# Performance work log

Hardware: AMD Instinct MI355X
Metric: run time of the kernel (lower is better)

Reference implementation:

```python
import jax, jax.numpy as jnp
import numpy as np

K = 3  # kernel_size

def setup_inputs() -> dict:
    key = jax.random.key(0)
    k0, k1, k2 = jax.random.split(key, 3)
    B, C, H, W = 8, 128, 128, 128
    x = jax.random.normal(k0, (B, C, H, W), dtype=jnp.float32)
    # kernel_gen params: two 1x1 convs acting on a 1x1 pooled map -> plain matmuls
    w1 = jax.random.normal(k1, (C, C), dtype=jnp.float32) * 0.05          # conv1 weight [out,in]
    b1 = jnp.zeros((C,), dtype=jnp.float32)
    w2 = jax.random.normal(k2, (C * K * K, C), dtype=jnp.float32) * 0.05  # conv2 weight [out,in]
    b2 = jnp.zeros((C * K * K,), dtype=jnp.float32)
    return {"x": x, "w1": w1, "b1": b1, "w2": w2, "b2": b2}

def reference(x, w1, b1, w2, b2):
    B, C, H, W = x.shape
    k = K
    pad = k // 2
    # AdaptiveAvgPool2d(1) -> global mean; 1x1 convs -> matmuls on [B, C]
    pooled = x.mean(axis=(2, 3))                        # [B, C]
    h = jax.nn.relu(pooled @ w1.T + b1)                 # [B, C]
    kern = (h @ w2.T + b2).reshape(B, C, k * k)         # [B, C, k*k], channel-major = reshape(B*C,1,k,k)
    # Dynamic per-sample depthwise conv (cross-correlation, zero pad), via patches
    patches = jax.lax.conv_general_dilated_patches(
        x, (k, k), (1, 1), ((pad, pad), (pad, pad)),
        dimension_numbers=("NCHW", "OIHW", "NCHW"))     # [B, C*k*k, H, W], channel-major over (C, k, k)
    patches = patches.reshape(B, C, k * k, H, W)
    out = jnp.einsum("bcphw,bcp->bchw", patches, kern)  # [B, C, H, W]
    return out
```

## Files before the change

kernel.cpp:

```cpp
#include <hip/hip_runtime.h>

#define BB 8
#define CC 128
#define HH 128
#define WW 128
#define PLANE (HH * WW)
#define KK 9

__global__ __launch_bounds__(256) void pool_kernel(const float* __restrict__ x,
                                                   float* __restrict__ pooled) {
    int bc = blockIdx.x;
    const float4* p4 = (const float4*)(x + (size_t)bc * PLANE);
    int t = threadIdx.x;
    float s = 0.f;
#pragma unroll
    for (int i = 0; i < 16; ++i) {
        float4 v = p4[t + i * 256];
        s += v.x + v.y + v.z + v.w;
    }
#pragma unroll
    for (int off = 32; off > 0; off >>= 1) s += __shfl_down(s, off, 64);
    __shared__ float wsum[4];
    int wave = t >> 6, lane = t & 63;
    if (lane == 0) wsum[wave] = s;
    __syncthreads();
    if (t == 0) {
        float tot = wsum[0] + wsum[1] + wsum[2] + wsum[3];
        pooled[bc] = tot * (1.0f / PLANE);
    }
}

__global__ __launch_bounds__(128) void kerngen_kernel(const float* __restrict__ pooled,
                                                      const float* __restrict__ w1,
                                                      const float* __restrict__ b1,
                                                      const float* __restrict__ w2,
                                                      const float* __restrict__ b2,
                                                      float* __restrict__ kern) {
    int b = blockIdx.x / 9;
    int g = blockIdx.x % 9;
    int j = threadIdx.x;
    __shared__ float ps[CC];
    __shared__ float hs[CC];
    ps[j] = pooled[b * CC + j];
    __syncthreads();
    float acc = b1[j];
    const float* w1r = w1 + j * CC;
#pragma unroll 8
    for (int i = 0; i < CC; ++i) acc += ps[i] * w1r[i];
    hs[j] = fmaxf(acc, 0.f);
    __syncthreads();
    int o = g * CC + j;
    float acc2 = b2[o];
    const float* w2r = w2 + o * CC;
#pragma unroll 8
    for (int i = 0; i < CC; ++i) acc2 += hs[i] * w2r[i];
    kern[b * (CC * KK) + o] = acc2;
}

__global__ __launch_bounds__(256) void conv_kernel(const float* __restrict__ x,
                                                   const float* __restrict__ kern,
                                                   float* __restrict__ out) {
    int bid = blockIdx.x;
    int bc = bid >> 2, slice = bid & 3;
    const float* plane = x + (size_t)bc * PLANE;
    float* oplane = out + (size_t)bc * PLANE;
    const float* wp = kern + (size_t)bc * KK;
    float w[9];
#pragma unroll
    for (int p = 0; p < 9; ++p) w[p] = wp[p];
    int t = threadIdx.x;
#pragma unroll
    for (int i = 0; i < 4; ++i) {
        int q = slice * 1024 + i * 256 + t;
        int y = q >> 5;
        int xq = q & 31;
        int x0 = xq << 2;
        float4 acc = {0.f, 0.f, 0.f, 0.f};
#pragma unroll
        for (int ky = 0; ky < 3; ++ky) {
            int yr = y + ky - 1;
            if (yr < 0 || yr >= HH) continue;
            const float* row = plane + yr * WW;
            float4 c = *(const float4*)(row + x0);
            float l = (x0 > 0) ? row[x0 - 1] : 0.f;
            float r = (xq < 31) ? row[x0 + 4] : 0.f;
            float w0 = w[ky * 3 + 0], w1_ = w[ky * 3 + 1], w2_ = w[ky * 3 + 2];
            acc.x += w0 * l   + w1_ * c.x + w2_ * c.y;
            acc.y += w0 * c.x + w1_ * c.y + w2_ * c.z;
            acc.z += w0 * c.y + w1_ * c.z + w2_ * c.w;
            acc.w += w0 * c.z + w1_ * c.w + w2_ * r;
        }
        *(float4*)(oplane + y * WW + x0) = acc;
    }
}

extern "C" void kernel_launch(void* const* d_in, const int* in_sizes, int n_in,
                              void* d_out, int out_size, void* d_ws, size_t ws_size,
                              hipStream_t stream) {
    const float* x  = (const float*)d_in[0];
    const float* w1 = (const float*)d_in[1];
    const float* b1 = (const float*)d_in[2];
    const float* w2 = (const float*)d_in[3];
    const float* b2 = (const float*)d_in[4];
    float* out = (float*)d_out;

    float* ws = (float*)d_ws;
    float* pooled = ws;
    float* kern   = ws + 1024;

    pool_kernel<<<BB * CC, 256, 0, stream>>>(x, pooled);
    kerngen_kernel<<<BB * 9, 128, 0, stream>>>(pooled, w1, b1, w2, b2, kern);
    conv_kernel<<<BB * CC * 4, 256, 0, stream>>>(x, kern, out);
}
```

Measured before the change: 146.8 us.

## Fuse kernel generation into depthwise conv with rolling row reuse

Removes the separate kernel-generation launch. Each conv block now recomputes the hidden vector and its own 9 taps from the pooled means, using shuffle reductions. The conv now gives each thread an 8-row strip and keeps rolling partial sums, so each input row is loaded once instead of three times. Each block redundantly recomputes the 128x128 first-layer matvec (1024 blocks), which adds L2 traffic and compute before the conv can start.

```diff
diff --git a/kernel.cpp b/kernel.cpp
--- a/kernel.cpp
+++ b/kernel.cpp
@@ -25,72 +25,99 @@
     if (lane == 0) wsum[wave] = s;
     __syncthreads();
     if (t == 0) {
-        float tot = wsum[0] + wsum[1] + wsum[2] + wsum[3];
-        pooled[bc] = tot * (1.0f / PLANE);
+        pooled[bc] = (wsum[0] + wsum[1] + wsum[2] + wsum[3]) * (1.0f / PLANE);
     }
 }
 
-__global__ __launch_bounds__(128) void kerngen_kernel(const float* __restrict__ pooled,
-                                                      const float* __restrict__ w1,
-                                                      const float* __restrict__ b1,
-                                                      const float* __restrict__ w2,
-                                                      const float* __restrict__ b2,
-                                                      float* __restrict__ kern) {
-    int b = blockIdx.x / 9;
-    int g = blockIdx.x % 9;
-    int j = threadIdx.x;
-    __shared__ float ps[CC];
+__global__ __launch_bounds__(512, 4) void fused_conv_kernel(
+        const float* __restrict__ x,
+        const float* __restrict__ pooled,
+        const float* __restrict__ w1,
+        const float* __restrict__ b1,
+        const float* __restrict__ w2,
+        const float* __restrict__ b2,
+        float* __restrict__ out) {
+    int bc = blockIdx.x;
+    int b = bc >> 7;
+    int c = bc & 127;
+    int t = threadIdx.x;
+
     __shared__ float hs[CC];
-    ps[j] = pooled[b * CC + j];
+    __shared__ float ks[KK];
+
+    {
+        int j = t >> 2;
+        int k = t & 3;
+        const float* pr = pooled + b * CC + k * 32;
+        const float* wr = w1 + j * CC + k * 32;
+        float a = 0.f;
+#pragma unroll
+        for (int i = 0; i < 32; ++i) a += pr[i] * wr[i];
+        a += __shfl_down(a, 1, 64);
+        a += __shfl_down(a, 2, 64);
+        if (k == 0) hs[j] = fmaxf(a + b1[j], 0.f);
+    }
     __syncthreads();
-    float acc = b1[j];
-    const float* w1r = w1 + j * CC;
-#pragma unroll 8
-    for (int i = 0; i < CC; ++i) acc += ps[i] * w1r[i];
-    hs[j] = fmaxf(acc, 0.f);
+
+    {
+        int w = t >> 6, lane = t & 63;
+        for (int p = w; p < KK; p += 8) {
+            int o = c * KK + p;
+            const float* wr = w2 + o * CC;
+            float a = hs[lane] * wr[lane] + hs[lane + 64] * wr[lane + 64];
+#pragma unroll
+            for (int off = 32; off > 0; off >>= 1) a += __shfl_down(a, off, 64);
+            if (lane == 0) ks[p] = a + b2[o];
+        }
+    }
     __syncthreads();
-    int o = g * CC + j;
-    float acc2 = b2[o];
-    const float* w2r = w2 + o * CC;
-#pragma unroll 8
-    for (int i = 0; i < CC; ++i) acc2 += hs[i] * w2r[i];
-    kern[b * (CC * KK) + o] = acc2;
-}
 
-__global__ __launch_bounds__(256) void conv_kernel(const float* __restrict__ x,
-                                                   const float* __restrict__ kern,
-                                                   float* __restrict__ out) {
-    int bid = blockIdx.x;
-    int bc = bid >> 2, slice = bid & 3;
+    float w[9];
+#pragma unroll
+    for (int p = 0; p < 9; ++p) w[p] = ks[p];
+
     const float* plane = x + (size_t)bc * PLANE;
     float* oplane = out + (size_t)bc * PLANE;
-    const float* wp = kern + (size_t)bc * KK;
-    float w[9];
+    int xq = t & 31;
+    int x0 = xq << 2;
+    int yb = (t >> 5) * 8;
+
+    float4 A = {0.f, 0.f, 0.f, 0.f};
+    float4 Bv = {0.f, 0.f, 0.f, 0.f};
+
 #pragma unroll
-    for (int p = 0; p < 9; ++p) w[p] = wp[p];
-    int t = threadIdx.x;
-#pragma unroll
-    for (int i = 0; i < 4; ++i) {
-        int q = slice * 1024 + i * 256 + t;
-        int y = q >> 5;
-        int xq = q & 31;
-        int x0 = xq << 2;
-        float4 acc = {0.f, 0.f, 0.f, 0.f};
-#pragma unroll
-        for (int ky = 0; ky < 3; ++ky) {
-            int yr = y + ky - 1;
-            if (yr < 0 || yr >= HH) continue;
+    for (int s = 0; s < 10; ++s) {
+        int yr = yb - 1 + s;
+        float4 cv = {0.f, 0.f, 0.f, 0.f};
+        float l = 0.f, r = 0.f;
+        if (yr >= 0 && yr < HH) {
             const float* row = plane + yr * WW;
-            float4 c = *(const float4*)(row + x0);
-            float l = (x0 > 0) ? row[x0 - 1] : 0.f;
-            float r = (xq < 31) ? row[x0 + 4] : 0.f;
-            float w0 = w[ky * 3 + 0], w1_ = w[ky * 3 + 1], w2_ = w[ky * 3 + 2];
-            acc.x += w0 * l   + w1_ * c.x + w2_ * c.y;
-            acc.y += w0 * c.x + w1_ * c.y + w2_ * c.z;
-            acc.z += w0 * c.y + w1_ * c.z + w2_ * c.w;
-            acc.w += w0 * c.z + w1_ * c.w + w2_ * r;
+            cv = *(const float4*)(row + x0);
+            l = (xq > 0) ? row[x0 - 1] : 0.f;
+            r = (xq < 31) ? row[x0 + 4] : 0.f;
         }
-        *(float4*)(oplane + y * WW + x0) = acc;
+        float4 pbot, pmid, ptop;
+        pbot.x = w[6]*l    + w[7]*cv.x + w[8]*cv.y;
+        pbot.y = w[6]*cv.x + w[7]*cv.y + w[8]*cv.z;
+        pbot.z = w[6]*cv.y + w[7]*cv.z + w[8]*cv.w;
+        pbot.w = w[6]*cv.z + w[7]*cv.w + w[8]*r;
+        pmid.x = w[3]*l    + w[4]*cv.x + w[5]*cv.y;
+        pmid.y = w[3]*cv.x + w[4]*cv.y + w[5]*cv.z;
+        pmid.z = w[3]*cv.y + w[4]*cv.z + w[5]*cv.w;
+        pmid.w = w[3]*cv.z + w[4]*cv.w + w[5]*r;
+        ptop.x = w[0]*l    + w[1]*cv.x + w[2]*cv.y;
+        ptop.y = w[0]*cv.x + w[1]*cv.y + w[2]*cv.z;
+        ptop.z = w[0]*cv.y + w[1]*cv.z + w[2]*cv.w;
+        ptop.w = w[0]*cv.z + w[1]*cv.w + w[2]*r;
+
+        A.x += pbot.x; A.y += pbot.y; A.z += pbot.z; A.w += pbot.w;
+        int yo = yr - 1;
+        if (yo >= yb && yo < yb + 8) {
+            *(float4*)(oplane + yo * WW + x0) = A;
+        }
+        Bv.x += pmid.x; Bv.y += pmid.y; Bv.z += pmid.z; Bv.w += pmid.w;
+        A = Bv;
+        Bv = ptop;
     }
 }
 
@@ -104,11 +131,8 @@
     const float* b2 = (const float*)d_in[4];
     float* out = (float*)d_out;
 
-    float* ws = (float*)d_ws;
-    float* pooled = ws;
-    float* kern   = ws + 1024;
+    float* pooled = (float*)d_ws;
 
     pool_kernel<<<BB * CC, 256, 0, stream>>>(x, pooled);
-    kerngen_kernel<<<BB * 9, 128, 0, stream>>>(pooled, w1, b1, w2, b2, kern);
-    conv_kernel<<<BB * CC * 4, 256, 0, stream>>>(x, kern, out);
+    fused_conv_kernel<<<BB * CC, 512, 0, stream>>>(x, pooled, w1, b1, w2, b2, out);
 }
```

Result: no change. 144.4 us (-1.7%).

## Slide a 3-row register window down 4 output rows in depthwise conv

Applied to the files above, without the earlier changes.

The conv kernel now gives each thread four consecutive output rows in one column quad. It loads 6 input rows once and accumulates partial sums in a rolling register window, where before each output row reloaded its 3 input rows. The pooling kernel also moves to 512 threads per block with 8 loads per thread. This is meant to cut redundant global/L2 loads in the conv, at the cost of more registers and a less regular store pattern.

```diff
diff --git a/kernel.cpp b/kernel.cpp
--- a/kernel.cpp
+++ b/kernel.cpp
@@ -7,25 +7,27 @@
 #define PLANE (HH * WW)
 #define KK 9
 
-__global__ __launch_bounds__(256) void pool_kernel(const float* __restrict__ x,
+__global__ __launch_bounds__(512) void pool_kernel(const float* __restrict__ x,
                                                    float* __restrict__ pooled) {
     int bc = blockIdx.x;
     const float4* p4 = (const float4*)(x + (size_t)bc * PLANE);
     int t = threadIdx.x;
     float s = 0.f;
 #pragma unroll
-    for (int i = 0; i < 16; ++i) {
-        float4 v = p4[t + i * 256];
+    for (int i = 0; i < 8; ++i) {
+        float4 v = p4[t + i * 512];
         s += v.x + v.y + v.z + v.w;
     }
 #pragma unroll
     for (int off = 32; off > 0; off >>= 1) s += __shfl_down(s, off, 64);
-    __shared__ float wsum[4];
+    __shared__ float wsum[8];
     int wave = t >> 6, lane = t & 63;
     if (lane == 0) wsum[wave] = s;
     __syncthreads();
     if (t == 0) {
-        float tot = wsum[0] + wsum[1] + wsum[2] + wsum[3];
+        float tot = 0.f;
+#pragma unroll
+        for (int i = 0; i < 8; ++i) tot += wsum[i];
         pooled[bc] = tot * (1.0f / PLANE);
     }
 }
@@ -68,29 +70,48 @@
     float w[9];
 #pragma unroll
     for (int p = 0; p < 9; ++p) w[p] = wp[p];
+
     int t = threadIdx.x;
+    int xq = t & 31;
+    int x0 = xq << 2;
+    int yb = slice * 32 + (t >> 5) * 4;
+
+    float4 A  = {0.f, 0.f, 0.f, 0.f};
+    float4 Bv = {0.f, 0.f, 0.f, 0.f};
+
 #pragma unroll
-    for (int i = 0; i < 4; ++i) {
-        int q = slice * 1024 + i * 256 + t;
-        int y = q >> 5;
-        int xq = q & 31;
-        int x0 = xq << 2;
-        float4 acc = {0.f, 0.f, 0.f, 0.f};
-#pragma unroll
-        for (int ky = 0; ky < 3; ++ky) {
-            int yr = y + ky - 1;
-            if (yr < 0 || yr >= HH) continue;
+    for (int s = 0; s < 6; ++s) {
+        int yr = yb - 1 + s;
+        float4 cv = {0.f, 0.f, 0.f, 0.f};
+        float l = 0.f, r = 0.f;
+        if (yr >= 0 && yr < HH) {
             const float* row = plane + yr * WW;
-            float4 c = *(const float4*)(row + x0);
-            float l = (x0 > 0) ? row[x0 - 1] : 0.f;
-            float r = (xq < 31) ? row[x0 + 4] : 0.f;
-            float w0 = w[ky * 3 + 0], w1_ = w[ky * 3 + 1], w2_ = w[ky * 3 + 2];
-            acc.x += w0 * l   + w1_ * c.x + w2_ * c.y;
-            acc.y += w0 * c.x + w1_ * c.y + w2_ * c.z;
-            acc.z += w0 * c.y + w1_ * c.z + w2_ * c.w;
-            acc.w += w0 * c.z + w1_ * c.w + w2_ * r;
+            cv = *(const float4*)(row + x0);
+            l = (xq > 0) ? row[x0 - 1] : 0.f;
+            r = (xq < 31) ? row[x0 + 4] : 0.f;
         }
-        *(float4*)(oplane + y * WW + x0) = acc;
+        float4 pbot, pmid, ptop;
+        pbot.x = w[6]*l    + w[7]*cv.x + w[8]*cv.y;
+        pbot.y = w[6]*cv.x + w[7]*cv.y + w[8]*cv.z;
+        pbot.z = w[6]*cv.y + w[7]*cv.z + w[8]*cv.w;
+        pbot.w = w[6]*cv.z + w[7]*cv.w + w[8]*r;
+        pmid.x = w[3]*l    + w[4]*cv.x + w[5]*cv.y;
+        pmid.y = w[3]*cv.x + w[4]*cv.y + w[5]*cv.z;
+        pmid.z = w[3]*cv.y + w[4]*cv.z + w[5]*cv.w;
+        pmid.w = w[3]*cv.z + w[4]*cv.w + w[5]*r;
+        ptop.x = w[0]*l    + w[1]*cv.x + w[2]*cv.y;
+        ptop.y = w[0]*cv.x + w[1]*cv.y + w[2]*cv.z;
+        ptop.z = w[0]*cv.y + w[1]*cv.z + w[2]*cv.w;
+        ptop.w = w[0]*cv.z + w[1]*cv.w + w[2]*r;
+
+        A.x += pbot.x; A.y += pbot.y; A.z += pbot.z; A.w += pbot.w;
+        int yo = yr - 1;
+        if (yo >= yb && yo < yb + 4) {
+            *(float4*)(oplane + yo * WW + x0) = A;
+        }
+        Bv.x += pmid.x; Bv.y += pmid.y; Bv.z += pmid.z; Bv.w += pmid.w;
+        A = Bv;
+        Bv = ptop;
     }
 }
 
@@ -108,7 +129,7 @@
     float* pooled = ws;
     float* kern   = ws + 1024;
 
-    pool_kernel<<<BB * CC, 256, 0, stream>>>(x, pooled);
+    pool_kernel<<<BB * CC, 512, 0, stream>>>(x, pooled);
     kerngen_kernel<<<BB * 9, 128, 0, stream>>>(pooled, w1, b1, w2, b2, kern);
     conv_kernel<<<BB * CC * 4, 256, 0, stream>>>(x, kern, out);
 }
```

After: 138.0 us. 6.0% less time.

## Register-tile conv rows per thread and use shuffles for halo columns

Applied to the files above, without the earlier changes.

The depthwise conv kernel now has each thread load a 10-row column strip of float4s into registers and compute 8 output rows from them. This reuses vertical neighbours instead of reloading each input row three times. Left and right halo values come from neighbouring lanes via width-32 shuffles instead of scalar global loads. The pool kernel moves to 512 threads with fewer iterations per thread. The cost is higher register pressure and half as many conv blocks.

```diff
diff --git a/kernel.cpp b/kernel.cpp
--- a/kernel.cpp
+++ b/kernel.cpp
@@ -7,25 +7,27 @@
 #define PLANE (HH * WW)
 #define KK 9
 
-__global__ __launch_bounds__(256) void pool_kernel(const float* __restrict__ x,
+__global__ __launch_bounds__(512) void pool_kernel(const float* __restrict__ x,
                                                    float* __restrict__ pooled) {
     int bc = blockIdx.x;
     const float4* p4 = (const float4*)(x + (size_t)bc * PLANE);
     int t = threadIdx.x;
     float s = 0.f;
 #pragma unroll
-    for (int i = 0; i < 16; ++i) {
-        float4 v = p4[t + i * 256];
+    for (int i = 0; i < 8; ++i) {
+        float4 v = p4[t + i * 512];
         s += v.x + v.y + v.z + v.w;
     }
 #pragma unroll
     for (int off = 32; off > 0; off >>= 1) s += __shfl_down(s, off, 64);
-    __shared__ float wsum[4];
+    __shared__ float wsum[8];
     int wave = t >> 6, lane = t & 63;
     if (lane == 0) wsum[wave] = s;
     __syncthreads();
     if (t == 0) {
-        float tot = wsum[0] + wsum[1] + wsum[2] + wsum[3];
+        float tot = 0.f;
+#pragma unroll
+        for (int i = 0; i < 8; ++i) tot += wsum[i];
         pooled[bc] = tot * (1.0f / PLANE);
     }
 }
@@ -61,36 +63,52 @@
                                                    const float* __restrict__ kern,
                                                    float* __restrict__ out) {
     int bid = blockIdx.x;
-    int bc = bid >> 2, slice = bid & 3;
-    const float* plane = x + (size_t)bc * PLANE;
+    int bc = bid >> 1, half = bid & 1;
+    const float* gplane = x + (size_t)bc * PLANE;
     float* oplane = out + (size_t)bc * PLANE;
     const float* wp = kern + (size_t)bc * KK;
     float w[9];
 #pragma unroll
     for (int p = 0; p < 9; ++p) w[p] = wp[p];
+
     int t = threadIdx.x;
+    int xq = t & 31;
+    int x0 = xq << 2;
+    int yb = half * 64 + (t >> 5) * 8;
+
+    float4 cv[10];
 #pragma unroll
-    for (int i = 0; i < 4; ++i) {
-        int q = slice * 1024 + i * 256 + t;
-        int y = q >> 5;
-        int xq = q & 31;
-        int x0 = xq << 2;
+    for (int si = 0; si < 10; ++si) {
+        int yr = yb - 1 + si;
+        if (yr >= 0 && yr < HH)
+            cv[si] = *(const float4*)(gplane + yr * WW + x0);
+        else
+            cv[si] = make_float4(0.f, 0.f, 0.f, 0.f);
+    }
+
+    float lv[10], rv[10];
+#pragma unroll
+    for (int si = 0; si < 10; ++si) {
+        float lraw = __shfl_up(cv[si].w, 1, 32);
+        float rraw = __shfl_down(cv[si].x, 1, 32);
+        lv[si] = (xq == 0) ? 0.f : lraw;
+        rv[si] = (xq == 31) ? 0.f : rraw;
+    }
+
+#pragma unroll
+    for (int o = 0; o < 8; ++o) {
         float4 acc = {0.f, 0.f, 0.f, 0.f};
 #pragma unroll
         for (int ky = 0; ky < 3; ++ky) {
-            int yr = y + ky - 1;
-            if (yr < 0 || yr >= HH) continue;
-            const float* row = plane + yr * WW;
-            float4 c = *(const float4*)(row + x0);
-            float l = (x0 > 0) ? row[x0 - 1] : 0.f;
-            float r = (xq < 31) ? row[x0 + 4] : 0.f;
-            float w0 = w[ky * 3 + 0], w1_ = w[ky * 3 + 1], w2_ = w[ky * 3 + 2];
-            acc.x += w0 * l   + w1_ * c.x + w2_ * c.y;
-            acc.y += w0 * c.x + w1_ * c.y + w2_ * c.z;
-            acc.z += w0 * c.y + w1_ * c.z + w2_ * c.w;
-            acc.w += w0 * c.z + w1_ * c.w + w2_ * r;
+            int si = o + ky;
+            float w0 = w[ky * 3], w1_ = w[ky * 3 + 1], w2_ = w[ky * 3 + 2];
+            float4 c = cv[si];
+            acc.x += w0 * lv[si] + w1_ * c.x + w2_ * c.y;
+            acc.y += w0 * c.x   + w1_ * c.y + w2_ * c.z;
+            acc.z += w0 * c.y   + w1_ * c.z + w2_ * c.w;
+            acc.w += w0 * c.z   + w1_ * c.w + w2_ * rv[si];
         }
-        *(float4*)(oplane + y * WW + x0) = acc;
+        *(float4*)(oplane + (yb + o) * WW + x0) = acc;
     }
 }
 
@@ -108,7 +126,7 @@
     float* pooled = ws;
     float* kern   = ws + 1024;
 
-    pool_kernel<<<BB * CC, 256, 0, stream>>>(x, pooled);
+    pool_kernel<<<BB * CC, 512, 0, stream>>>(x, pooled);
     kerngen_kernel<<<BB * 9, 128, 0, stream>>>(pooled, w1, b1, w2, b2, kern);
-    conv_kernel<<<BB * CC * 4, 256, 0, stream>>>(x, kern, out);
+    conv_kernel<<<BB * CC * 2, 256, 0, stream>>>(x, kern, out);
 }
```

After: 134.5 us. 8.4% less time.
